# Kernel tuning notes

Measured on AMD Instinct MI355X. Metric: run time of the kernel, lower is better.

The kernel has to match this reference:

```python
import jax, jax.numpy as jnp
import numpy as np

NUM_USERS = 100000
NUM_ITEMS = 50000
DIM_H = 64
NUM_LAYERS = 4
NUM_EDGES = 2000000


def setup_inputs() -> dict:
    key = jax.random.key(0)
    k1, k2, k3, k4 = jax.random.split(key, 4)
    emb_users = jax.random.normal(k1, (NUM_USERS, DIM_H), dtype=jnp.float32) * 0.01
    emb_items = jax.random.normal(k2, (NUM_ITEMS, DIM_H), dtype=jnp.float32) * 0.01
    edge_users = jax.random.randint(k3, (NUM_EDGES,), 0, NUM_USERS, dtype=jnp.int64)
    edge_items = jax.random.randint(k4, (NUM_EDGES,), 0, NUM_ITEMS, dtype=jnp.int64)
    edge_values = jnp.ones((NUM_EDGES,), dtype=jnp.float32)
    return {"emb_users": emb_users, "emb_items": emb_items,
            "edge_users": edge_users, "edge_items": edge_items,
            "edge_values": edge_values}


def reference(emb_users, emb_items, edge_users, edge_items, edge_values):
    U = emb_users.shape[0]
    I = emb_items.shape[0]
    N = U + I
    # Symmetric bipartite adjacency in COO form: (u, i+U) and (i+U, u).
    rows = jnp.concatenate([edge_users, edge_items + U])
    cols = jnp.concatenate([edge_items + U, edge_users])
    vals = jnp.concatenate([edge_values, edge_values])
    # D^{-1/2} A D^{-1/2} normalization (inf -> 0 for isolated nodes).
    deg = jax.ops.segment_sum(vals, rows, num_segments=N)
    dinv = jnp.where(deg > 0, jax.lax.rsqrt(jnp.maximum(deg, 1e-12)), 0.0)
    nvals = dinv[rows] * vals * dinv[cols]

    emb = jnp.concatenate([emb_users, emb_items])  # [N, d]
    acc = emb  # running sum over layer outputs (incl. layer 0)
    e = emb
    for _ in range(NUM_LAYERS):
        # SpMM: e <- A_norm @ e via gather + segment-sum scatter
        e = jax.ops.segment_sum(nvals[:, None] * e[cols], rows, num_segments=N)
        acc = acc + e
    alpha = 1.0 / (NUM_LAYERS + 1)
    # Original computes alpha * mean(stack(embs)), i.e. sum / (L+1)^2.
    emb_final = alpha * (acc / (NUM_LAYERS + 1))
    embf_users = emb_final[:U]
    embf_items = emb_final[U:]
    return (embf_users, emb_users, embf_items, emb_items)
```

## Files before the change

### kernel.cpp

```cpp
#include <hip/hip_runtime.h>


static inline size_t align_up(size_t x, size_t a) { return (x + a - 1) & ~(a - 1); }

#define NBA 640
#define KB  1024

__device__ inline unsigned short f32_to_bf16(float f) {
    unsigned int u = __float_as_uint(f);
    unsigned int r = (u + 0x7FFFu + ((u >> 16) & 1u)) >> 16;
    return (unsigned short)r;
}
__device__ inline float bf16_to_f32(unsigned short h) {
    return __uint_as_float(((unsigned int)h) << 16);
}
__device__ inline float bf16_lo(unsigned int d) {
    return __uint_as_float(d << 16);
}
__device__ inline float bf16_hi(unsigned int d) {
    return __uint_as_float(d & 0xFFFF0000u);
}

__global__ __launch_bounds__(256) void k_bucket_count(
        const int* __restrict__ eu, const int* __restrict__ ei,
        int* __restrict__ bh, int U, int E, int NB, int CH) {
    __shared__ int hist[NBA];
    int k = blockIdx.x;
    int t = threadIdx.x;
    for (int b = t; b < NBA; b += 256) hist[b] = 0;
    __syncthreads();
    int lo = k * CH, hi = min(E, lo + CH);
    for (int i = lo + t; i < hi; i += 256) {
        int u  = eu[i];
        int it = ei[i] + U;
        atomicAdd(&hist[u >> 8], 1);
        atomicAdd(&hist[it >> 8], 1);
    }
    __syncthreads();
    for (int b = t; b < NB; b += 256) bh[k * NBA + b] = hist[b];
}

__global__ __launch_bounds__(256) void k_scan_blocks(
        int* __restrict__ bh, int* __restrict__ total, int NB) {
    __shared__ int s[256];
    int b = blockIdx.x;
    int t = threadIdx.x;
    int k0 = t * 4;
    int vals[4];
    int sum = 0;
    #pragma unroll
    for (int j = 0; j < 4; ++j) { vals[j] = bh[(k0 + j) * NBA + b]; sum += vals[j]; }
    s[t] = sum;
    __syncthreads();
    for (int d = 1; d < 256; d <<= 1) {
        int v = (t >= d) ? s[t - d] : 0;
        __syncthreads();
        s[t] += v;
        __syncthreads();
    }
    int run = s[t] - sum;
    #pragma unroll
    for (int j = 0; j < 4; ++j) { int v = vals[j]; bh[(k0 + j) * NBA + b] = run; run += v; }
    if (t == 255) total[b] = run;
}

__global__ __launch_bounds__(256) void k_scan_buckets(
        const int* __restrict__ total, int* __restrict__ bbase, int NB) {
    __shared__ int s[256];
    int t = threadIdx.x;
    int C = (NB + 255) / 256;
    int vals[4];
    int sum = 0;
    for (int j = 0; j < C; ++j) {
        int idx = t * C + j;
        int v = (idx < NB) ? total[idx] : 0;
        vals[j] = v; sum += v;
    }
    s[t] = sum;
    __syncthreads();
    for (int d = 1; d < 256; d <<= 1) {
        int v = (t >= d) ? s[t - d] : 0;
        __syncthreads();
        s[t] += v;
        __syncthreads();
    }
    int run = s[t] - sum;
    for (int j = 0; j < C; ++j) {
        int idx = t * C + j;
        if (idx < NB) bbase[idx] = run;
        run += vals[j];
    }
}

__global__ __launch_bounds__(256) void k_bucket_scatter(
        const int* __restrict__ eu, const int* __restrict__ ei,
        const float* __restrict__ ev, const int* __restrict__ bh,
        int2* __restrict__ gb, int U, int E, int NB, int CH, int CAP) {
    __shared__ int lbase[NBA];
    int k = blockIdx.x;
    int t = threadIdx.x;
    for (int b = t; b < NB; b += 256) lbase[b] = b * CAP + bh[k * NBA + b];
    __syncthreads();
    int lo = k * CH, hi = min(E, lo + CH);
    for (int i = lo + t; i < hi; i += 256) {
        int u  = eu[i];
        int it = ei[i] + U;
        int vb = __float_as_int(ev[i]);
        int b1 = u >> 8;
        int p1 = atomicAdd(&lbase[b1], 1);
        if (p1 < (b1 + 1) * CAP) gb[p1] = make_int2((u & 255) | (it << 8), vb);
        int b2 = it >> 8;
        int p2 = atomicAdd(&lbase[b2], 1);
        if (p2 < (b2 + 1) * CAP) gb[p2] = make_int2((it & 255) | (u << 8), vb);
    }
}

__global__ __launch_bounds__(256) void k_bucket_csr(
        const int2* __restrict__ gb, const int* __restrict__ total,
        const int* __restrict__ bbase,
        int* __restrict__ offs, int* __restrict__ cnt,
        float* __restrict__ dinv, float* __restrict__ dsq,
        int2* __restrict__ csr, int N, int CAP) {
    __shared__ int   hist[256];
    __shared__ float degf[256];
    __shared__ int   offl[256];
    __shared__ int   scan[256];
    int b = blockIdx.x;
    int t = threadIdx.x;
    int n0 = b << 8;
    int nbc = min(256, N - n0);
    int cb = min(total[b], CAP);
    int base = bbase[b];
    const int2* gbb = gb + (size_t)b * CAP;

    hist[t] = 0;
    degf[t] = 0.f;
    __syncthreads();
    for (int i = t; i < cb; i += 256) {
        int2 e = gbb[i];
        int rl = e.x & 255;
        atomicAdd(&hist[rl], 1);
        atomicAdd(&degf[rl], __int_as_float(e.y));
    }
    __syncthreads();
    int h = hist[t];
    scan[t] = h;
    __syncthreads();
    for (int d = 1; d < 256; d <<= 1) {
        int v = (t >= d) ? scan[t - d] : 0;
        __syncthreads();
        scan[t] += v;
        __syncthreads();
    }
    offl[t] = scan[t] - h;
    if (t < nbc) {
        int node = n0 + t;
        offs[node] = base + (scan[t] - h);
        cnt[node]  = h;
        float s = degf[t];
        bool pos = (s > 0.0f);
        dinv[node] = pos ? rsqrtf(fmaxf(s, 1e-12f)) : 0.0f;
        dsq[node]  = pos ? sqrtf(s) : 0.0f;
    }
    hist[t] = 0;
    __syncthreads();
    for (int i = t; i < cb; i += 256) {
        int2 e = gbb[i];
        int rl = e.x & 255;
        int col = (int)(((unsigned)e.x) >> 8);
        int tk = atomicAdd(&hist[rl], 1);
        csr[base + offl[rl] + tk] = make_int2(col, e.y);
    }
}

__global__ void k_init(const float4* __restrict__ emb_u, const float4* __restrict__ emb_i,
                       const float* __restrict__ dinv,
                       ushort4* __restrict__ g0, int U16, int N16) {
    int i = blockIdx.x * blockDim.x + threadIdx.x;
    if (i >= N16) return;
    float4 v = (i < U16) ? emb_u[i] : emb_i[i - U16];
    float d = dinv[i >> 4];
    ushort4 o;
    o.x = f32_to_bf16(v.x * d);
    o.y = f32_to_bf16(v.y * d);
    o.z = f32_to_bf16(v.z * d);
    o.w = f32_to_bf16(v.w * d);
    g0[i] = o;
}

__global__ __launch_bounds__(256) void k_layer(
        const uint4* __restrict__ gin, uint4* __restrict__ gout,
        const float* __restrict__ dinv,
        const int* __restrict__ offs, const int* __restrict__ cnt,
        const int2* __restrict__ csr, int N) {
    int gtid = blockIdx.x * blockDim.x + threadIdx.x;
    int row = gtid >> 6;
    int lane = threadIdx.x & 63;
    if (row >= N) return;
    int nb = lane >> 3;
    int q  = lane & 7;
    int base = offs[row];
    int c = cnt[row];

    float a0 = 0.f, a1 = 0.f, a2 = 0.f, a3 = 0.f;
    float a4 = 0.f, a5 = 0.f, a6 = 0.f, a7 = 0.f;

    for (int k0 = 0; k0 < c; k0 += 64) {
        int idx = k0 + lane;
        int2 cw = make_int2(0, 0);
        if (idx < c) cw = csr[base + idx];
        int m = min(c - k0, 64);
        int j = 0;
        for (; j + 16 <= m; j += 16) {
            int   colA = __shfl(cw.x, j + nb);
            float wA   = __int_as_float(__shfl(cw.y, j + nb));
            int   colB = __shfl(cw.x, j + 8 + nb);
            float wB   = __int_as_float(__shfl(cw.y, j + 8 + nb));
            uint4 gA = gin[(size_t)colA * 8 + q];
            uint4 gB = gin[(size_t)colB * 8 + q];
            a0 += wA * bf16_lo(gA.x); a1 += wA * bf16_hi(gA.x);
            a2 += wA * bf16_lo(gA.y); a3 += wA * bf16_hi(gA.y);
            a4 += wA * bf16_lo(gA.z); a5 += wA * bf16_hi(gA.z);
            a6 += wA * bf16_lo(gA.w); a7 += wA * bf16_hi(gA.w);
            a0 += wB * bf16_lo(gB.x); a1 += wB * bf16_hi(gB.x);
            a2 += wB * bf16_lo(gB.y); a3 += wB * bf16_hi(gB.y);
            a4 += wB * bf16_lo(gB.z); a5 += wB * bf16_hi(gB.z);
            a6 += wB * bf16_lo(gB.w); a7 += wB * bf16_hi(gB.w);
        }
        for (; j < m; j += 8) {
            int   col = __shfl(cw.x, j + nb);
            float w   = __int_as_float(__shfl(cw.y, j + nb));
            uint4 gv = gin[(size_t)col * 8 + q];
            a0 += w * bf16_lo(gv.x); a1 += w * bf16_hi(gv.x);
            a2 += w * bf16_lo(gv.y); a3 += w * bf16_hi(gv.y);
            a4 += w * bf16_lo(gv.z); a5 += w * bf16_hi(gv.z);
            a6 += w * bf16_lo(gv.w); a7 += w * bf16_hi(gv.w);
        }
    }

    #pragma unroll
    for (int mask = 8; mask <= 32; mask <<= 1) {
        a0 += __shfl_xor(a0, mask); a1 += __shfl_xor(a1, mask);
        a2 += __shfl_xor(a2, mask); a3 += __shfl_xor(a3, mask);
        a4 += __shfl_xor(a4, mask); a5 += __shfl_xor(a5, mask);
        a6 += __shfl_xor(a6, mask); a7 += __shfl_xor(a7, mask);
    }

    if (nb == 0) {
        float dr = dinv[row];
        float d2 = dr * dr;
        uint4 o;
        o.x = (unsigned int)f32_to_bf16(d2 * a0) | ((unsigned int)f32_to_bf16(d2 * a1) << 16);
        o.y = (unsigned int)f32_to_bf16(d2 * a2) | ((unsigned int)f32_to_bf16(d2 * a3) << 16);
        o.z = (unsigned int)f32_to_bf16(d2 * a4) | ((unsigned int)f32_to_bf16(d2 * a5) << 16);
        o.w = (unsigned int)f32_to_bf16(d2 * a6) | ((unsigned int)f32_to_bf16(d2 * a7) << 16);
        gout[(size_t)row * 8 + q] = o;
    }
}

__global__ void k_final(const float4* __restrict__ emb_u, const float4* __restrict__ emb_i,
                        const ushort4* __restrict__ g1, const ushort4* __restrict__ g2,
                        const ushort4* __restrict__ g3, const ushort4* __restrict__ g4,
                        const float* __restrict__ dsq,
                        float4* __restrict__ out, int U16, int I16) {
    int i = blockIdx.x * blockDim.x + threadIdx.x;
    int total = 2 * U16 + 2 * I16;
    if (i >= total) return;
    const float s = 1.0f / 25.0f;
    float4 r;
    if (i < U16 || (i >= 2 * U16 && i < 2 * U16 + I16)) {
        int gi, node;
        float4 e0;
        if (i < U16) { gi = i; node = i >> 4; e0 = emb_u[i]; }
        else { int j = i - 2 * U16; gi = U16 + j; node = (U16 >> 4) + (j >> 4); e0 = emb_i[j]; }
        float d = dsq[node];
        ushort4 a = g1[gi], b = g2[gi], cc = g3[gi], dd = g4[gi];
        float gx = bf16_to_f32(a.x) + bf16_to_f32(b.x) + bf16_to_f32(cc.x) + bf16_to_f32(dd.x);
        float gy = bf16_to_f32(a.y) + bf16_to_f32(b.y) + bf16_to_f32(cc.y) + bf16_to_f32(dd.y);
        float gz = bf16_to_f32(a.z) + bf16_to_f32(b.z) + bf16_to_f32(cc.z) + bf16_to_f32(dd.z);
        float gw = bf16_to_f32(a.w) + bf16_to_f32(b.w) + bf16_to_f32(cc.w) + bf16_to_f32(dd.w);
        r = make_float4((e0.x + d * gx) * s, (e0.y + d * gy) * s,
                        (e0.z + d * gz) * s, (e0.w + d * gw) * s);
    } else if (i < 2 * U16) {
        r = emb_u[i - U16];
    } else {
        r = emb_i[i - 2 * U16 - I16];
    }
    out[i] = r;
}

extern "C" void kernel_launch(void* const* d_in, const int* in_sizes, int n_in,
                              void* d_out, int out_size, void* d_ws, size_t ws_size,
                              hipStream_t stream) {
    const float* emb_u = (const float*)d_in[0];
    const float* emb_i = (const float*)d_in[1];
    const int*   eu    = (const int*)d_in[2];
    const int*   ei    = (const int*)d_in[3];
    const float* ev    = (const float*)d_in[4];

    const int U = in_sizes[0] / 64;
    const int I = in_sizes[1] / 64;
    const int N = U + I;
    const int E = in_sizes[2];
    const int DE = 2 * E;

    const int NB = (N + 255) >> 8;
    const int CH = (E + KB - 1) / KB;

    char* base = (char*)d_ws;
    size_t off = 0;
    int*   offs  = (int*)  (base + off); off = align_up(off + (size_t)N * 4, 256);
    int*   cnt   = (int*)  (base + off); off = align_up(off + (size_t)N * 4, 256);
    float* dinv  = (float*)(base + off); off = align_up(off + (size_t)N * 4, 256);
    float* dsq   = (float*)(base + off); off = align_up(off + (size_t)N * 4, 256);
    int*   bh    = (int*)  (base + off); off = align_up(off + (size_t)NBA * KB * 4, 256);
    int*   total = (int*)  (base + off); off = align_up(off + (size_t)NBA * 4, 256);
    int*   bbase = (int*)  (base + off); off = align_up(off + (size_t)NBA * 4, 256);
    int2*  csr   = (int2*) (base + off); off = align_up(off + (size_t)DE * 8, 256);
    unsigned short* g[5];
    for (int l = 0; l < 5; ++l) {
        g[l] = (unsigned short*)(base + off);
        off = align_up(off + (size_t)N * 64 * 2, 256);
    }
    (void)ws_size;

    int2* gb = (int2*)g[1];
    size_t gcap = (size_t)4 * N * 128;
    int CAP = (int)(gcap / ((size_t)NB * 8));
    if (CAP > 16128) CAP = 16128;

    const int B = 256;
    k_bucket_count  <<<KB, B, 0, stream>>>(eu, ei, bh, U, E, NB, CH);
    k_scan_blocks   <<<NB, B, 0, stream>>>(bh, total, NB);
    k_scan_buckets  <<<1,  B, 0, stream>>>(total, bbase, NB);
    k_bucket_scatter<<<KB, B, 0, stream>>>(eu, ei, ev, bh, gb, U, E, NB, CH, CAP);
    k_bucket_csr    <<<NB, B, 0, stream>>>(gb, total, bbase, offs, cnt, dinv, dsq, csr, N, CAP);

    const int U16 = U * 16, I16 = I * 16, N16 = N * 16;
    k_init<<<(N16 + B - 1) / B, B, 0, stream>>>((const float4*)emb_u, (const float4*)emb_i,
                                                dinv, (ushort4*)g[0], U16, N16);

    for (int layer = 0; layer < 4; ++layer) {
        int threads = N * 64;
        k_layer<<<(threads + B - 1) / B, B, 0, stream>>>(
            (const uint4*)g[layer], (uint4*)g[layer + 1], dinv, offs, cnt, csr, N);
    }

    int totalv4 = 2 * U16 + 2 * I16;
    k_final<<<(totalv4 + B - 1) / B, B, 0, stream>>>(
        (const float4*)emb_u, (const float4*)emb_i,
        (const ushort4*)g[1], (const ushort4*)g[2], (const ushort4*)g[3], (const ushort4*)g[4],
        dsq, (float4*)d_out, U16, I16);
}
```

Before: 589.9 us.

## Use 8 lanes per row in SpMM with 4-padded CSR and prefetch

Each row is now handled by 8 lanes instead of a 64-lane wavefront, which removes the shuffle broadcast of edge entries and the cross-lane reduction. CSR segments are padded to multiples of 4 with zero-weight entries, so each thread reads 4 edges as two 16-byte loads and prefetches the next group while it gathers the current one. Bucket bases get extra slack and the workspace is enlarged to hold the padding. The cost is more padding memory, and every lane of a row now walks the whole edge list serially, which raises per-thread latency for rows with many edges.

```diff
diff --git a/kernel.cpp b/kernel.cpp
--- a/kernel.cpp
+++ b/kernel.cpp
@@ -73,7 +73,7 @@
     int sum = 0;
     for (int j = 0; j < C; ++j) {
         int idx = t * C + j;
-        int v = (idx < NB) ? total[idx] : 0;
+        int v = (idx < NB) ? (((total[idx] + 3) & ~3) + 768) : 0;
         vals[j] = v; sum += v;
     }
     s[t] = sum;
@@ -144,7 +144,8 @@
     }
     __syncthreads();
     int h = hist[t];
-    scan[t] = h;
+    int h4 = (h + 3) & ~3;
+    scan[t] = h4;
     __syncthreads();
     for (int d = 1; d < 256; d <<= 1) {
         int v = (t >= d) ? scan[t - d] : 0;
@@ -152,15 +153,18 @@
         scan[t] += v;
         __syncthreads();
     }
-    offl[t] = scan[t] - h;
+    int off4 = scan[t] - h4;
+    offl[t] = off4;
     if (t < nbc) {
         int node = n0 + t;
-        offs[node] = base + (scan[t] - h);
+        offs[node] = base + off4;
         cnt[node]  = h;
         float s = degf[t];
         bool pos = (s > 0.0f);
         dinv[node] = pos ? rsqrtf(fmaxf(s, 1e-12f)) : 0.0f;
         dsq[node]  = pos ? sqrtf(s) : 0.0f;
+        for (int p = h; p < h4; ++p)
+            csr[base + off4 + p] = make_int2(0, 0);
     }
     hist[t] = 0;
     __syncthreads();
@@ -194,68 +198,58 @@
         const int* __restrict__ offs, const int* __restrict__ cnt,
         const int2* __restrict__ csr, int N) {
     int gtid = blockIdx.x * blockDim.x + threadIdx.x;
-    int row = gtid >> 6;
-    int lane = threadIdx.x & 63;
+    int row = gtid >> 3;
+    unsigned q = threadIdx.x & 7;
     if (row >= N) return;
-    int nb = lane >> 3;
-    int q  = lane & 7;
     int base = offs[row];
     int c = cnt[row];
+    int nIter = (c + 3) >> 2;
 
     float a0 = 0.f, a1 = 0.f, a2 = 0.f, a3 = 0.f;
     float a4 = 0.f, a5 = 0.f, a6 = 0.f, a7 = 0.f;
 
-    for (int k0 = 0; k0 < c; k0 += 64) {
-        int idx = k0 + lane;
-        int2 cw = make_int2(0, 0);
-        if (idx < c) cw = csr[base + idx];
-        int m = min(c - k0, 64);
-        int j = 0;
-        for (; j + 16 <= m; j += 16) {
-            int   colA = __shfl(cw.x, j + nb);
-            float wA   = __int_as_float(__shfl(cw.y, j + nb));
-            int   colB = __shfl(cw.x, j + 8 + nb);
-            float wB   = __int_as_float(__shfl(cw.y, j + 8 + nb));
-            uint4 gA = gin[(size_t)colA * 8 + q];
-            uint4 gB = gin[(size_t)colB * 8 + q];
-            a0 += wA * bf16_lo(gA.x); a1 += wA * bf16_hi(gA.x);
-            a2 += wA * bf16_lo(gA.y); a3 += wA * bf16_hi(gA.y);
-            a4 += wA * bf16_lo(gA.z); a5 += wA * bf16_hi(gA.z);
-            a6 += wA * bf16_lo(gA.w); a7 += wA * bf16_hi(gA.w);
-            a0 += wB * bf16_lo(gB.x); a1 += wB * bf16_hi(gB.x);
-            a2 += wB * bf16_lo(gB.y); a3 += wB * bf16_hi(gB.y);
-            a4 += wB * bf16_lo(gB.z); a5 += wB * bf16_hi(gB.z);
-            a6 += wB * bf16_lo(gB.w); a7 += wB * bf16_hi(gB.w);
-        }
-        for (; j < m; j += 8) {
-            int   col = __shfl(cw.x, j + nb);
-            float w   = __int_as_float(__shfl(cw.y, j + nb));
-            uint4 gv = gin[(size_t)col * 8 + q];
-            a0 += w * bf16_lo(gv.x); a1 += w * bf16_hi(gv.x);
-            a2 += w * bf16_lo(gv.y); a3 += w * bf16_hi(gv.y);
-            a4 += w * bf16_lo(gv.z); a5 += w * bf16_hi(gv.z);
-            a6 += w * bf16_lo(gv.w); a7 += w * bf16_hi(gv.w);
-        }
-    }
-
-    #pragma unroll
-    for (int mask = 8; mask <= 32; mask <<= 1) {
-        a0 += __shfl_xor(a0, mask); a1 += __shfl_xor(a1, mask);
-        a2 += __shfl_xor(a2, mask); a3 += __shfl_xor(a3, mask);
-        a4 += __shfl_xor(a4, mask); a5 += __shfl_xor(a5, mask);
-        a6 += __shfl_xor(a6, mask); a7 += __shfl_xor(a7, mask);
-    }
-
-    if (nb == 0) {
-        float dr = dinv[row];
-        float d2 = dr * dr;
-        uint4 o;
-        o.x = (unsigned int)f32_to_bf16(d2 * a0) | ((unsigned int)f32_to_bf16(d2 * a1) << 16);
-        o.y = (unsigned int)f32_to_bf16(d2 * a2) | ((unsigned int)f32_to_bf16(d2 * a3) << 16);
-        o.z = (unsigned int)f32_to_bf16(d2 * a4) | ((unsigned int)f32_to_bf16(d2 * a5) << 16);
-        o.w = (unsigned int)f32_to_bf16(d2 * a6) | ((unsigned int)f32_to_bf16(d2 * a7) << 16);
-        gout[(size_t)row * 8 + q] = o;
-    }
+    const uint4* ep4 = (const uint4*)(csr + base);
+    uint4 E0 = make_uint4(0, 0, 0, 0), E1 = E0;
+    if (nIter > 0) { E0 = ep4[0]; E1 = ep4[1]; }
+
+    for (int i = 0; i < nIter; ++i) {
+        uint4 G0 = gin[(E0.x << 3) | q];
+        uint4 G1 = gin[(E0.z << 3) | q];
+        uint4 G2 = gin[(E1.x << 3) | q];
+        uint4 G3 = gin[(E1.z << 3) | q];
+        uint4 P0 = ep4[2 * i + 2];
+        uint4 P1 = ep4[2 * i + 3];
+        float w0 = __uint_as_float(E0.y);
+        float w1 = __uint_as_float(E0.w);
+        float w2 = __uint_as_float(E1.y);
+        float w3 = __uint_as_float(E1.w);
+        a0 += w0 * bf16_lo(G0.x); a1 += w0 * bf16_hi(G0.x);
+        a2 += w0 * bf16_lo(G0.y); a3 += w0 * bf16_hi(G0.y);
+        a4 += w0 * bf16_lo(G0.z); a5 += w0 * bf16_hi(G0.z);
+        a6 += w0 * bf16_lo(G0.w); a7 += w0 * bf16_hi(G0.w);
+        a0 += w1 * bf16_lo(G1.x); a1 += w1 * bf16_hi(G1.x);
+        a2 += w1 * bf16_lo(G1.y); a3 += w1 * bf16_hi(G1.y);
+        a4 += w1 * bf16_lo(G1.z); a5 += w1 * bf16_hi(G1.z);
+        a6 += w1 * bf16_lo(G1.w); a7 += w1 * bf16_hi(G1.w);
+        a0 += w2 * bf16_lo(G2.x); a1 += w2 * bf16_hi(G2.x);
+        a2 += w2 * bf16_lo(G2.y); a3 += w2 * bf16_hi(G2.y);
+        a4 += w2 * bf16_lo(G2.z); a5 += w2 * bf16_hi(G2.z);
+        a6 += w2 * bf16_lo(G2.w); a7 += w2 * bf16_hi(G2.w);
+        a0 += w3 * bf16_lo(G3.x); a1 += w3 * bf16_hi(G3.x);
+        a2 += w3 * bf16_lo(G3.y); a3 += w3 * bf16_hi(G3.y);
+        a4 += w3 * bf16_lo(G3.z); a5 += w3 * bf16_hi(G3.z);
+        a6 += w3 * bf16_lo(G3.w); a7 += w3 * bf16_hi(G3.w);
+        E0 = P0; E1 = P1;
+    }
+
+    float dr = dinv[row];
+    float d2 = dr * dr;
+    uint4 o;
+    o.x = (unsigned int)f32_to_bf16(d2 * a0) | ((unsigned int)f32_to_bf16(d2 * a1) << 16);
+    o.y = (unsigned int)f32_to_bf16(d2 * a2) | ((unsigned int)f32_to_bf16(d2 * a3) << 16);
+    o.z = (unsigned int)f32_to_bf16(d2 * a4) | ((unsigned int)f32_to_bf16(d2 * a5) << 16);
+    o.w = (unsigned int)f32_to_bf16(d2 * a6) | ((unsigned int)f32_to_bf16(d2 * a7) << 16);
+    gout[((unsigned)row << 3) | q] = o;
 }
 
 __global__ void k_final(const float4* __restrict__ emb_u, const float4* __restrict__ emb_i,
@@ -316,7 +310,8 @@
     int*   bh    = (int*)  (base + off); off = align_up(off + (size_t)NBA * KB * 4, 256);
     int*   total = (int*)  (base + off); off = align_up(off + (size_t)NBA * 4, 256);
     int*   bbase = (int*)  (base + off); off = align_up(off + (size_t)NBA * 4, 256);
-    int2*  csr   = (int2*) (base + off); off = align_up(off + (size_t)DE * 8, 256);
+    int2*  csr   = (int2*) (base + off);
+    off = align_up(off + ((size_t)DE + (size_t)NBA * 772 + 16) * 8, 256);
     unsigned short* g[5];
     for (int l = 0; l < 5; ++l) {
         g[l] = (unsigned short*)(base + off);
@@ -341,7 +336,7 @@
                                                 dinv, (ushort4*)g[0], U16, N16);
 
     for (int layer = 0; layer < 4; ++layer) {
-        int threads = N * 64;
+        int threads = N * 8;
         k_layer<<<(threads + B - 1) / B, B, 0, stream>>>(
             (const uint4*)g[layer], (uint4*)g[layer + 1], dinv, offs, cnt, csr, N);
     }
```

Result: faster. 545.5 us (-7.5%).
